# Kernel optimization log

Hardware: AMD Instinct MI355X
Metric: run time of the kernel (lower is better)

## Reference

```python
import jax, jax.numpy as jnp
import numpy as np

# size_ranges buffer from the module (17 keypoints, [min,max] fractional size)
SIZE_RANGES = np.array(
    [[0.1, 0.2]] * 5 + [[0.15, 0.3]] * 2 + [[0.1, 0.25]] * 2 + [[0.1, 0.2]] * 2
    + [[0.2, 0.4]] * 2 + [[0.15, 0.3]] * 2 + [[0.1, 0.25]] * 2,
    dtype=np.float32)

PATCH = 30  # base patch resolution after nearest upsample of 3x3 texture


def _bilinear_zeros(img, gx, gy):
    """torch.grid_sample(bilinear, zeros padding, align_corners=False).
    img: [C,h,w]; gx,gy: [H,W] normalized coords in [-1,1]. Returns [C,H,W]."""
    C, h, w = img.shape
    ix = ((gx + 1.0) * w - 1.0) * 0.5
    iy = ((gy + 1.0) * h - 1.0) * 0.5
    ix0 = jnp.floor(ix)
    iy0 = jnp.floor(iy)
    wx1 = ix - ix0
    wy1 = iy - iy0

    def gather(iyf, ixf):
        valid = ((ixf >= 0) & (ixf <= w - 1) & (iyf >= 0) & (iyf <= h - 1)).astype(img.dtype)
        ii = jnp.clip(ixf, 0, w - 1).astype(jnp.int32)
        jj = jnp.clip(iyf, 0, h - 1).astype(jnp.int32)
        return img[:, jj, ii] * valid  # [C,H,W]

    return (gather(iy0, ix0) * (1 - wy1) * (1 - wx1)
            + gather(iy0, ix0 + 1) * (1 - wy1) * wx1
            + gather(iy0 + 1, ix0) * wy1 * (1 - wx1)
            + gather(iy0 + 1, ix0 + 1) * wy1 * wx1)


def setup_inputs() -> dict:
    key = jax.random.key(0)
    ks = jax.random.split(key, 8)
    B, P, K, H, W = 2, 4, 17, 512, 512
    images = jax.random.normal(ks[0], (B, 3, H, W), jnp.float32)
    kx = jax.random.uniform(ks[1], (B, P, K)) * W
    ky = jax.random.uniform(ks[2], (B, P, K)) * H
    kv = jax.random.randint(ks[3], (B, P, K), 0, 3).astype(jnp.float32)
    targets_keypoints = jnp.stack([kx, ky, kv], axis=-1)  # [B,P,K,3]
    bx = jax.random.uniform(ks[4], (B, P)) * W
    by = jax.random.uniform(ks[5], (B, P)) * H
    bw = 50.0 + jax.random.uniform(ks[6], (B, P)) * 250.0
    targets_bboxes = jnp.stack([bx, by, bw, bw], axis=-1)  # [B,P,4]
    grid_texture = jax.random.normal(ks[7], (K, 1, 3, 3), jnp.float32)
    size_logits = jnp.zeros((K,), jnp.float32)
    alpha_logits = jnp.ones((K,), jnp.float32)
    return dict(images=images, targets_keypoints=targets_keypoints,
                targets_bboxes=targets_bboxes, grid_texture=grid_texture,
                size_logits=size_logits, alpha_logits=alpha_logits)


def reference(images, targets_keypoints, targets_bboxes, grid_texture, size_logits, alpha_logits):
    B, C, H, W = images.shape
    K = grid_texture.shape[0]
    # binary-ish texture, nearest-upsampled 3x3 -> 30x30 (repeat factor 10)
    bw_tex = jax.nn.sigmoid(grid_texture * 10.0)                 # [K,1,3,3]
    base = jnp.repeat(jnp.repeat(bw_tex, 10, axis=-2), 10, axis=-1)  # [K,1,30,30]
    base3 = jnp.broadcast_to(base, (K, 3, PATCH, PATCH))
    sr = jnp.asarray(SIZE_RANGES)
    actual_scales = sr[:, 0] + jax.nn.sigmoid(size_logits) * (sr[:, 1] - sr[:, 0])
    alphas = jax.nn.sigmoid(alpha_logits)
    # affine_grid(align_corners=False) base coordinates
    base_x = (2.0 * jnp.arange(W) + 1.0) / W - 1.0  # [W]
    base_y = (2.0 * jnp.arange(H) + 1.0) / H - 1.0  # [H]
    ones_patch = jnp.ones((1, PATCH, PATCH), images.dtype)

    def warp_kp(patch, x, y, v, person_w, s_factor, alpha):
        valid = ((v != 0) & (person_w > 1.0)).astype(images.dtype)
        pps = jnp.maximum(s_factor * person_w, 3.0)  # clamp(min=3)
        inv_sx = W / pps
        inv_sy = H / pps
        nx = x / W * 2.0 - 1.0
        ny = y / H * 2.0 - 1.0
        gx = jnp.broadcast_to((base_x - nx) * inv_sx, (H, W))
        gy = jnp.broadcast_to(((base_y - ny) * inv_sy)[:, None], (H, W))
        pw = _bilinear_zeros(patch, gx, gy)            # [3,H,W]
        mw = _bilinear_zeros(ones_patch, gx, gy)[0]    # [H,W]
        return pw, mw * alpha * valid

    warp_k = jax.vmap(warp_kp, in_axes=(0, 0, 0, 0, None, 0, 0))          # over K
    warp_pk = jax.vmap(warp_k, in_axes=(None, 0, 0, 0, 0, None, None))    # over P
    warp_bpk = jax.vmap(warp_pk, in_axes=(None, 0, 0, 0, 0, None, None))  # over B

    kx = targets_keypoints[..., 0]
    ky = targets_keypoints[..., 1]
    kv = targets_keypoints[..., 2]
    person_w = targets_bboxes[..., 2]
    pw, me = warp_bpk(base3, kx, ky, kv, person_w, actual_scales, alphas)
    # pw: [B,P,K,3,H,W], me: [B,P,K,H,W]
    P = kx.shape[1]
    S = P * K
    pws = pw.reshape(B, S, C, H, W).transpose(1, 0, 2, 3, 4)        # [S,B,3,H,W]
    mes = me.reshape(B, S, H, W).transpose(1, 0, 2, 3)[:, :, None]  # [S,B,1,H,W]

    def step(img, xs):
        p, m = xs
        return img * (1.0 - m) + p * m, None

    out, _ = jax.lax.scan(step, images, (pws, mes))
    return out, alphas
```

## Files before the change

kernel.cpp:

```cpp
#include <hip/hip_runtime.h>

#define HH 512
#define WW 512
#define NB 2
#define NP 4
#define NK 17
#define NS (NP*NK)

__constant__ float c_sr[NK*2] = {
  0.10f,0.20f, 0.10f,0.20f, 0.10f,0.20f, 0.10f,0.20f, 0.10f,0.20f,
  0.15f,0.30f, 0.15f,0.30f,
  0.10f,0.25f, 0.10f,0.25f,
  0.10f,0.20f, 0.10f,0.20f,
  0.20f,0.40f, 0.20f,0.40f,
  0.15f,0.30f, 0.15f,0.30f,
  0.10f,0.25f, 0.10f,0.25f
};


__global__ __launch_bounds__(256) void setup_k(
    const float* __restrict__ kpts,
    const float* __restrict__ bbox,
    const float* __restrict__ gtex,
    const float* __restrict__ slog,
    const float* __restrict__ alog,
    float* __restrict__ ws,
    float* __restrict__ alphas_out)
{
  int tid = threadIdx.x;
  if (tid < NK*9) {
    ws[tid] = 1.0f / (1.0f + expf(-10.0f * gtex[tid]));
  }
  if (tid < NK) {
    alphas_out[tid] = 1.0f / (1.0f + expf(-alog[tid]));
  }
  if (tid < NB*NS) {
    int b = tid / NS, s = tid % NS, p = s / NK, k = s % NK;
    const float* kp = kpts + ((b*NP + p)*NK + k)*3;
    float x = kp[0], y = kp[1], v = kp[2];
    float pw = bbox[(b*NP + p)*4 + 2];
    float sig   = 1.0f / (1.0f + expf(-slog[k]));
    float sc    = c_sr[2*k] + sig * (c_sr[2*k+1] - c_sr[2*k]);
    float alpha = 1.0f / (1.0f + expf(-alog[k]));
    float valid = (v != 0.0f && pw > 1.0f) ? 1.0f : 0.0f;
    float pps = fmaxf(sc * pw, 3.0f);
    float fx = 30.0f / pps;
    float4 pr;
    pr.x = fx;
    pr.y = fx * (0.5f - x) + 14.5f;
    pr.z = fx * (0.5f - y) + 14.5f;
    pr.w = alpha * valid;
    reinterpret_cast<float4*>(ws + 160)[tid] = pr;
  }
  __syncthreads();
  if (tid < NB) {
    const float4* raw = reinterpret_cast<const float4*>(ws + 160) + tid*NS;
    float4* cp = reinterpret_cast<float4*>(ws + 720) + tid*NS;
    int* ck = reinterpret_cast<int*>(ws) + 1264 + tid*NS;
    int cnt = 0;
    for (int s = 0; s < NS; ++s) {
      float4 pr = raw[s];
      if (pr.w > 0.0f) {
        cp[cnt] = pr;
        ck[cnt] = (s % NK) * 9;
        cnt++;
      }
    }
    reinterpret_cast<int*>(ws)[704 + tid] = cnt;
  }
}

__global__ __launch_bounds__(256) void comp_k(
    const float* __restrict__ images, const float* __restrict__ ws,
    float* __restrict__ out)
{
  __shared__ float  s_tex[NK*9];
  __shared__ float4 s_par[NS];
  __shared__ int    s_kid[NS];
  __shared__ float4 s_cp[NS];
  __shared__ int    s_ck[NS];
  __shared__ int    s_cnt;

  int tid = threadIdx.x;
  int gid = blockIdx.x * 256 + tid;
  int b   = gid >> 18;
  int pix = gid & (HH*WW - 1);
  int cnt_g = reinterpret_cast<const int*>(ws)[704 + b];

  if (tid < NK*9) s_tex[tid] = ws[tid];
  if (tid < NS) {
    s_par[tid] = reinterpret_cast<const float4*>(ws + 720)[b*NS + tid];
    s_kid[tid] = reinterpret_cast<const int*>(ws)[1264 + b*NS + tid];
  }
  __syncthreads();

  int i = pix >> 9;
  int j = pix & (WW - 1);

  if (tid < 64) {
    float rowf  = (float)i;
    float jminf = (float)((blockIdx.x & 1) * 256);
    float jmaxf = jminf + 255.0f;
    bool pred = false;
    if (tid < cnt_g) {
      float4 pr = s_par[tid];
      float iy  = fmaf(pr.x, rowf,  pr.z);
      float ixa = fmaf(pr.x, jminf, pr.y);
      float ixb = fmaf(pr.x, jmaxf, pr.y);
      pred = (iy > -1.0f) && (iy < 30.0f) && (ixb > -1.0f) && (ixa < 30.0f);
    }
    unsigned long long m1 = __ballot(pred);
    int rank = __popcll(m1 & ((1ull << tid) - 1ull));
    if (pred) { s_cp[rank] = s_par[tid]; s_ck[rank] = s_kid[tid]; }
    int base = __popcll(m1);
    bool pred2 = false;
    int s2 = 64 + tid;
    if (s2 < cnt_g) {
      float4 pr = s_par[s2];
      float iy  = fmaf(pr.x, rowf,  pr.z);
      float ixa = fmaf(pr.x, jminf, pr.y);
      float ixb = fmaf(pr.x, jmaxf, pr.y);
      pred2 = (iy > -1.0f) && (iy < 30.0f) && (ixb > -1.0f) && (ixa < 30.0f);
    }
    unsigned long long m2 = __ballot(pred2);
    int rank2 = base + __popcll(m2 & ((1ull << tid) - 1ull));
    if (pred2) { s_cp[rank2] = s_par[s2]; s_ck[rank2] = s_kid[s2]; }
    if (tid == 0) s_cnt = base + __popcll(m2);
  }
  __syncthreads();
  int nact = s_cnt;

  const float* ib = images + b*(3*HH*WW) + pix;
  float r0 = ib[0];
  float r1 = ib[HH*WW];
  float r2 = ib[2*HH*WW];
  float jf = (float)j, if_ = (float)i;

  for (int n = 0; n < nact; ++n) {
    float4 pr = s_cp[n];
    float ix = fmaf(pr.x, jf,  pr.y);
    float iy = fmaf(pr.x, if_, pr.z);
    if (ix > -1.0f && ix < 30.0f && iy > -1.0f && iy < 30.0f) {
      int toff = s_ck[n];
      float ix0f = floorf(ix), iy0f = floorf(iy);
      float wx1 = ix - ix0f, wy1 = iy - iy0f;
      float wx0 = 1.0f - wx1, wy0 = 1.0f - wy1;
      int x0 = (int)ix0f, y0 = (int)iy0f;
      int x1 = x0 + 1, y1 = y0 + 1;
      bool vx0 = (unsigned)x0 < 30u;
      bool vx1 = (unsigned)x1 < 30u;
      bool vy0 = (unsigned)y0 < 30u;
      bool vy1 = (unsigned)y1 < 30u;
      int cx0 = x0 >= 20 ? 2 : (x0 >= 10 ? 1 : 0);
      int cx1 = x1 >= 20 ? 2 : (x1 >= 10 ? 1 : 0);
      int cy0 = y0 >= 20 ? 6 : (y0 >= 10 ? 3 : 0);
      int cy1 = y1 >= 20 ? 6 : (y1 >= 10 ? 3 : 0);
      const float* tk = s_tex + toff;
      float mw = 0.0f, pv = 0.0f, w;
      w = (vx0 && vy0) ? wy0*wx0 : 0.0f; mw += w; pv = fmaf(w, tk[cy0+cx0], pv);
      w = (vx1 && vy0) ? wy0*wx1 : 0.0f; mw += w; pv = fmaf(w, tk[cy0+cx1], pv);
      w = (vx0 && vy1) ? wy1*wx0 : 0.0f; mw += w; pv = fmaf(w, tk[cy1+cx0], pv);
      w = (vx1 && vy1) ? wy1*wx1 : 0.0f; mw += w; pv = fmaf(w, tk[cy1+cx1], pv);
      float m  = mw * pr.w;
      float om = 1.0f - m;
      float pm = pv * m;
      r0 = fmaf(r0, om, pm);
      r1 = fmaf(r1, om, pm);
      r2 = fmaf(r2, om, pm);
    }
  }
  float* ob = out + b*(3*HH*WW) + pix;
  ob[0]        = r0;
  ob[HH*WW]    = r1;
  ob[2*HH*WW]  = r2;
}

extern "C" void kernel_launch(void* const* d_in, const int* in_sizes, int n_in,
                              void* d_out, int out_size, void* d_ws, size_t ws_size,
                              hipStream_t stream) {
  const float* images = (const float*)d_in[0];
  const float* kpts   = (const float*)d_in[1];
  const float* bbox   = (const float*)d_in[2];
  const float* gtex   = (const float*)d_in[3];
  const float* slog   = (const float*)d_in[4];
  const float* alog   = (const float*)d_in[5];
  float* outp = (float*)d_out;
  float* ws   = (float*)d_ws;
  float* alphas_out = outp + NB*3*HH*WW;

  hipLaunchKernelGGL(setup_k, dim3(1), dim3(256), 0, stream,
                     kpts, bbox, gtex, slog, alog, ws, alphas_out);
  hipLaunchKernelGGL(comp_k, dim3((NB*HH*WW)/256), dim3(256), 0, stream,
                     images, ws, outp);
}
```

Measured before the change: 83.98 us.

## Fuse setup kernel into compositing kernel, recomputing parameters per block

Removes the single-block setup kernel and its workspace round trip. Each compositing block now recomputes the sigmoid texture weights and the per-keypoint affine parameters straight into shared memory, using threads 188..255 for its batch's 68 keypoints. Validity is folded into the per-row ballot compaction instead of a serial pre-compaction. This saves a kernel launch and the serialized setup latency, at the cost of redundant transcendental math and scattered global loads in every block.

```diff
diff --git a/kernel.cpp b/kernel.cpp
--- a/kernel.cpp
+++ b/kernel.cpp
@@ -17,25 +17,37 @@
   0.10f,0.25f, 0.10f,0.25f
 };
 
-
-__global__ __launch_bounds__(256) void setup_k(
+__global__ __launch_bounds__(256) void fused_k(
+    const float* __restrict__ images,
     const float* __restrict__ kpts,
     const float* __restrict__ bbox,
     const float* __restrict__ gtex,
     const float* __restrict__ slog,
     const float* __restrict__ alog,
-    float* __restrict__ ws,
+    float* __restrict__ out,
     float* __restrict__ alphas_out)
 {
+  __shared__ float  s_tex[NK*9];
+  __shared__ float4 s_par[NS];
+  __shared__ float4 s_cp[NS];
+  __shared__ int    s_ck[NS];
+  __shared__ int    s_cnt;
+
   int tid = threadIdx.x;
+  int gid = blockIdx.x * 256 + tid;
+  int b   = gid >> 18;
+  int pix = gid & (HH*WW - 1);
+
   if (tid < NK*9) {
-    ws[tid] = 1.0f / (1.0f + expf(-10.0f * gtex[tid]));
+    s_tex[tid] = 1.0f / (1.0f + __expf(-10.0f * gtex[tid]));
   }
-  if (tid < NK) {
-    alphas_out[tid] = 1.0f / (1.0f + expf(-alog[tid]));
+  if (blockIdx.x == 0 && tid >= 160 && tid < 160 + NK) {
+    int k = tid - 160;
+    alphas_out[k] = 1.0f / (1.0f + expf(-alog[k]));
   }
-  if (tid < NB*NS) {
-    int b = tid / NS, s = tid % NS, p = s / NK, k = s % NK;
+  if (tid >= 188) {
+    int s = tid - 188;
+    int p = s / NK, k = s - p*NK;
     const float* kp = kpts + ((b*NP + p)*NK + k)*3;
     float x = kp[0], y = kp[1], v = kp[2];
     float pw = bbox[(b*NP + p)*4 + 2];
@@ -50,47 +62,7 @@
     pr.y = fx * (0.5f - x) + 14.5f;
     pr.z = fx * (0.5f - y) + 14.5f;
     pr.w = alpha * valid;
-    reinterpret_cast<float4*>(ws + 160)[tid] = pr;
-  }
-  __syncthreads();
-  if (tid < NB) {
-    const float4* raw = reinterpret_cast<const float4*>(ws + 160) + tid*NS;
-    float4* cp = reinterpret_cast<float4*>(ws + 720) + tid*NS;
-    int* ck = reinterpret_cast<int*>(ws) + 1264 + tid*NS;
-    int cnt = 0;
-    for (int s = 0; s < NS; ++s) {
-      float4 pr = raw[s];
-      if (pr.w > 0.0f) {
-        cp[cnt] = pr;
-        ck[cnt] = (s % NK) * 9;
-        cnt++;
-      }
-    }
-    reinterpret_cast<int*>(ws)[704 + tid] = cnt;
-  }
-}
-
-__global__ __launch_bounds__(256) void comp_k(
-    const float* __restrict__ images, const float* __restrict__ ws,
-    float* __restrict__ out)
-{
-  __shared__ float  s_tex[NK*9];
-  __shared__ float4 s_par[NS];
-  __shared__ int    s_kid[NS];
-  __shared__ float4 s_cp[NS];
-  __shared__ int    s_ck[NS];
-  __shared__ int    s_cnt;
-
-  int tid = threadIdx.x;
-  int gid = blockIdx.x * 256 + tid;
-  int b   = gid >> 18;
-  int pix = gid & (HH*WW - 1);
-  int cnt_g = reinterpret_cast<const int*>(ws)[704 + b];
-
-  if (tid < NK*9) s_tex[tid] = ws[tid];
-  if (tid < NS) {
-    s_par[tid] = reinterpret_cast<const float4*>(ws + 720)[b*NS + tid];
-    s_kid[tid] = reinterpret_cast<const int*>(ws)[1264 + b*NS + tid];
+    s_par[s] = pr;
   }
   __syncthreads();
 
@@ -101,30 +73,30 @@
     float rowf  = (float)i;
     float jminf = (float)((blockIdx.x & 1) * 256);
     float jmaxf = jminf + 255.0f;
-    bool pred = false;
-    if (tid < cnt_g) {
-      float4 pr = s_par[tid];
-      float iy  = fmaf(pr.x, rowf,  pr.z);
-      float ixa = fmaf(pr.x, jminf, pr.y);
-      float ixb = fmaf(pr.x, jmaxf, pr.y);
-      pred = (iy > -1.0f) && (iy < 30.0f) && (ixb > -1.0f) && (ixa < 30.0f);
-    }
+    float4 pr = s_par[tid];
+    float iy  = fmaf(pr.x, rowf,  pr.z);
+    float ixa = fmaf(pr.x, jminf, pr.y);
+    float ixb = fmaf(pr.x, jmaxf, pr.y);
+    bool pred = (pr.w > 0.0f) && (iy > -1.0f) && (iy < 30.0f)
+              && (ixb > -1.0f) && (ixa < 30.0f);
     unsigned long long m1 = __ballot(pred);
     int rank = __popcll(m1 & ((1ull << tid) - 1ull));
-    if (pred) { s_cp[rank] = s_par[tid]; s_ck[rank] = s_kid[tid]; }
+    int kk = (int)((unsigned)tid % (unsigned)NK);
+    if (pred) { s_cp[rank] = pr; s_ck[rank] = kk*9; }
     int base = __popcll(m1);
     bool pred2 = false;
     int s2 = 64 + tid;
-    if (s2 < cnt_g) {
-      float4 pr = s_par[s2];
-      float iy  = fmaf(pr.x, rowf,  pr.z);
-      float ixa = fmaf(pr.x, jminf, pr.y);
-      float ixb = fmaf(pr.x, jmaxf, pr.y);
-      pred2 = (iy > -1.0f) && (iy < 30.0f) && (ixb > -1.0f) && (ixa < 30.0f);
+    if (s2 < NS) {
+      float4 q = s_par[s2];
+      float iy2  = fmaf(q.x, rowf,  q.z);
+      float ixa2 = fmaf(q.x, jminf, q.y);
+      float ixb2 = fmaf(q.x, jmaxf, q.y);
+      pred2 = (q.w > 0.0f) && (iy2 > -1.0f) && (iy2 < 30.0f)
+            && (ixb2 > -1.0f) && (ixa2 < 30.0f);
     }
     unsigned long long m2 = __ballot(pred2);
     int rank2 = base + __popcll(m2 & ((1ull << tid) - 1ull));
-    if (pred2) { s_cp[rank2] = s_par[s2]; s_ck[rank2] = s_kid[s2]; }
+    if (pred2) { s_cp[rank2] = s_par[s2]; s_ck[rank2] = ((s2 - 51) % NK) * 9; }
     if (tid == 0) s_cnt = base + __popcll(m2);
   }
   __syncthreads();
@@ -185,11 +157,8 @@
   const float* slog   = (const float*)d_in[4];
   const float* alog   = (const float*)d_in[5];
   float* outp = (float*)d_out;
-  float* ws   = (float*)d_ws;
   float* alphas_out = outp + NB*3*HH*WW;
 
-  hipLaunchKernelGGL(setup_k, dim3(1), dim3(256), 0, stream,
-                     kpts, bbox, gtex, slog, alog, ws, alphas_out);
-  hipLaunchKernelGGL(comp_k, dim3((NB*HH*WW)/256), dim3(256), 0, stream,
-                     images, ws, outp);
+  hipLaunchKernelGGL(fused_k, dim3((NB*HH*WW)/256), dim3(256), 0, stream,
+                     images, kpts, bbox, gtex, slog, alog, outp, alphas_out);
 }
```

New measurement: 69.89 us. -16.8%, faster.
